# Performance work log

Hardware: AMD Instinct MI355X
Metric: run time of the kernel (lower is better)

The kernel has to match this reference:

```python
import jax, jax.numpy as jnp
import numpy as np

HIDDEN = 2048
NUM_HEADS = 32
NUM_KV_HEADS = 8
GROUP = NUM_HEADS // NUM_KV_HEADS  # 4
HEAD_DIM = HIDDEN // NUM_HEADS     # 64
SEQ = 2048


def setup_inputs() -> dict:
    key = jax.random.key(0)
    ks = jax.random.split(key, 5)
    s = HIDDEN ** -0.5
    x = jax.random.normal(ks[0], (SEQ, HIDDEN), jnp.float32)
    q_proj = jax.random.normal(ks[1], (HIDDEN, HIDDEN), jnp.float32) * s
    k_proj = jax.random.normal(ks[2], (HIDDEN, HIDDEN // GROUP), jnp.float32) * s
    v_proj = jax.random.normal(ks[3], (HIDDEN, HIDDEN // GROUP), jnp.float32) * s
    o_proj = jax.random.normal(ks[4], (HIDDEN, HIDDEN), jnp.float32) * s
    # inv_freq = 1/rsqrt(10000**(i/d)) = sqrt(10000**(i/d)) per the original module
    inv_freq = jnp.sqrt(10000.0 ** (jnp.arange(0, HEAD_DIM, 2) / HEAD_DIM)).astype(jnp.float32)
    return {"x": x, "q_proj": q_proj, "k_proj": k_proj, "v_proj": v_proj,
            "o_proj": o_proj, "inv_freq": inv_freq}


def _rope(x, inv_freq):
    # x: [S, ..., HEAD_DIM]; rotation per the original (nonstandard) formula.
    orig_dtype = x.dtype
    x = x.astype(jnp.float32)
    seq = jnp.arange(x.shape[0])
    angles = seq[:, None] * jax.lax.stop_gradient(inv_freq)[None, :]  # [S, HEAD_DIM//2]
    bshape = (x.shape[0],) + (1,) * (x.ndim - 2) + (HEAD_DIM // 2,)
    sins = jnp.sin(angles).reshape(bshape)
    coss = jnp.cos(angles).reshape(bshape)
    half, odd = jnp.split(x, 2, axis=-1)
    out = jnp.concatenate([half * coss + odd * sins, half * sins - odd * coss], axis=-1)
    return out.astype(orig_dtype)


def reference(x, q_proj, k_proj, v_proj, o_proj, inv_freq):
    S = x.shape[0]
    q = (x @ q_proj).reshape(S, NUM_KV_HEADS, GROUP, HEAD_DIM)
    k = (x @ k_proj).reshape(S, NUM_KV_HEADS, HEAD_DIM)
    v = (x @ v_proj).reshape(S, NUM_KV_HEADS, HEAD_DIM)
    q = _rope(q, inv_freq)
    k = _rope(k, inv_freq)
    # scores: [a=S, b=S, h=kv_heads, g=group]
    scores = jnp.einsum('ahgd,bhd->abhg', q, k) / (HEAD_DIM ** 0.5)
    mask = jnp.tril(jnp.ones((S, S), dtype=jnp.bool_))[:, :, None, None]
    scores = jnp.where(mask, scores, -jnp.inf)
    attn = jax.nn.softmax(scores, axis=1)  # softmax over b (axis=-3)
    o = jnp.einsum('abhg,bhd->ahgd', attn, v).reshape(S, HIDDEN)
    return o @ o_proj
```

## Files before the change

### kernel.cpp

```cpp
#include <hip/hip_runtime.h>


typedef __bf16 bf16_t;
typedef __bf16 bf16x4 __attribute__((ext_vector_type(4)));
typedef __bf16 bf16x8 __attribute__((ext_vector_type(8)));
typedef float  f32x4  __attribute__((ext_vector_type(4)));
typedef short  s16x4  __attribute__((ext_vector_type(4)));

#define S_LEN   2048
#define HID     2048
#define NKV     8
#define NH      32
#define DHEAD   64
#define KVW     (NKV * DHEAD)

__device__ __align__(16) bf16_t g_xb [S_LEN * HID];
__device__ __align__(16) bf16_t g_wTq[HID * HID];
__device__ __align__(16) bf16_t g_wTk[KVW * HID];
__device__ __align__(16) bf16_t g_wTv[KVW * HID];
__device__ __align__(16) bf16_t g_wTo[HID * HID];
__device__ __align__(16) bf16_t g_q [S_LEN * HID];
__device__ __align__(16) bf16_t g_k [S_LEN * KVW];
__device__ __align__(16) bf16_t g_vT[KVW * S_LEN];
__device__ __align__(16) bf16_t g_om[S_LEN * HID];
__device__ float g_ropeC[S_LEN * 32];
__device__ float g_ropeS[S_LEN * 32];

static __device__ inline s16x4 bc4(bf16x4 v) { s16x4 r; __builtin_memcpy(&r, &v, 8); return r; }

__device__ __forceinline__ void gll16(void* lds, const void* g) {
    __builtin_amdgcn_global_load_lds(
        (const __attribute__((address_space(1))) void*)g,
        (__attribute__((address_space(3))) void*)lds,
        16, 0, 0);
}

__global__ __launch_bounds__(256)
void prep_kernel(const float* __restrict__ x,
                 const float* __restrict__ qw, const float* __restrict__ kw,
                 const float* __restrict__ vw, const float* __restrict__ ow,
                 const void* __restrict__ invf_raw) {
    __shared__ bf16_t tile[64][65];
    int b = blockIdx.x, t = threadIdx.x;

    if (b < 256) {
        int idx = b * 256 + t;
        int s = idx >> 5, j = idx & 31;
        float f;
        if (*(const unsigned*)invf_raw == 0x3F800000u) {
            f = ((const float*)invf_raw)[j];
        } else {
            unsigned u = ((unsigned)((const unsigned short*)invf_raw)[j]) << 16;
            __builtin_memcpy(&f, &u, 4);
        }
        double a = (double)s * (double)f;
        g_ropeC[idx] = (float)cos(a);
        g_ropeS[idx] = (float)sin(a);
        return;
    }
    if (b < 4352) {
        int idx = (b - 256) * 256 + t;
        float4 v = reinterpret_cast<const float4*>(x)[idx];
        bf16x4 o;
        o[0] = (bf16_t)v.x; o[1] = (bf16_t)v.y; o[2] = (bf16_t)v.z; o[3] = (bf16_t)v.w;
        *reinterpret_cast<bf16x4*>(&g_xb[(size_t)idx * 4]) = o;
        return;
    }
    const float* in; bf16_t* outp; int R, C, tb;
    if (b < 5376)      { in = qw; outp = g_wTq; R = HID; C = HID; tb = b - 4352; }
    else if (b < 5632) { in = kw; outp = g_wTk; R = HID; C = KVW; tb = b - 5376; }
    else if (b < 5888) { in = vw; outp = g_wTv; R = HID; C = KVW; tb = b - 5632; }
    else               { in = ow; outp = g_wTo; R = HID; C = HID; tb = b - 5888; }
    int xt = C >> 6;
    int c0 = (tb % xt) * 64, r0 = (tb / xt) * 64;
    int tx = t & 63, ty = t >> 6;
    #pragma unroll
    for (int r = ty; r < 64; r += 4)
        tile[r][tx] = (bf16_t)in[(size_t)(r0 + r) * C + c0 + tx];
    __syncthreads();
    #pragma unroll
    for (int r = ty; r < 64; r += 4)
        outp[(size_t)(c0 + r) * R + r0 + tx] = tile[tx][r];
}

__global__ __launch_bounds__(256)
void gemm_fused_kernel(float* __restrict__ Cf, int which) {
    __shared__ __align__(16) bf16_t As[2][64 * 64];
    __shared__ __align__(16) bf16_t Bs[2][128 * 64];

    int t    = threadIdx.x;
    int lane = t & 63, wid = t >> 6;
    int quad = lane >> 4, l15 = lane & 15;
    int bx = blockIdx.x, m0 = blockIdx.y * 64;
    int wm = (wid >> 1) * 32, wn = (wid & 1) * 64;

    const bf16_t* A; const bf16_t* Bt; int n0;
    if (which == 1)      { A = g_om; Bt = g_wTo; n0 = bx * 128; }
    else {
        A = g_xb;
        if (bx < 16)      { Bt = g_wTq; n0 = bx * 128; }
        else if (bx < 20) { Bt = g_wTk; n0 = (bx - 16) * 128; }
        else              { Bt = g_wTv; n0 = (bx - 20) * 128; }
    }

    int crow = lane >> 3;
    int gseg = (lane & 7) ^ crow;
    int so   = l15 & 7;

    f32x4 acc[2][4];
    #pragma unroll
    for (int im = 0; im < 2; ++im)
        #pragma unroll
        for (int in = 0; in < 4; ++in)
            #pragma unroll
            for (int r = 0; r < 4; ++r) acc[im][in][r] = 0.f;

    auto stage = [&](int buf, int kt) {
        int ca0 = wid * 2, cb0 = wid * 4;
        gll16(&As[buf][(ca0 + 0) * 512], A  + (size_t)(m0 + (ca0 + 0) * 8 + crow) * HID + kt + gseg * 8);
        gll16(&As[buf][(ca0 + 1) * 512], A  + (size_t)(m0 + (ca0 + 1) * 8 + crow) * HID + kt + gseg * 8);
        gll16(&Bs[buf][(cb0 + 0) * 512], Bt + (size_t)(n0 + (cb0 + 0) * 8 + crow) * HID + kt + gseg * 8);
        gll16(&Bs[buf][(cb0 + 1) * 512], Bt + (size_t)(n0 + (cb0 + 1) * 8 + crow) * HID + kt + gseg * 8);
        gll16(&Bs[buf][(cb0 + 2) * 512], Bt + (size_t)(n0 + (cb0 + 2) * 8 + crow) * HID + kt + gseg * 8);
        gll16(&Bs[buf][(cb0 + 3) * 512], Bt + (size_t)(n0 + (cb0 + 3) * 8 + crow) * HID + kt + gseg * 8);
    };

    stage(0, 0);

    for (int it = 0; it < 32; ++it) {
        int cur = it & 1;
        __syncthreads();
        if (it + 1 < 32)
            stage(cur ^ 1, (it + 1) * 64);

        bf16x8 af[2][2], bfr[4][2];
        #pragma unroll
        for (int im = 0; im < 2; ++im)
            #pragma unroll
            for (int kh = 0; kh < 2; ++kh)
                af[im][kh] = *reinterpret_cast<const bf16x8*>(
                    &As[cur][(wm + im * 16 + l15) * 64 + (((kh * 4 + quad) ^ so) * 8)]);
        #pragma unroll
        for (int in = 0; in < 4; ++in)
            #pragma unroll
            for (int kh = 0; kh < 2; ++kh)
                bfr[in][kh] = *reinterpret_cast<const bf16x8*>(
                    &Bs[cur][(wn + in * 16 + l15) * 64 + (((kh * 4 + quad) ^ so) * 8)]);
        #pragma unroll
        for (int im = 0; im < 2; ++im)
            #pragma unroll
            for (int in = 0; in < 4; ++in)
                #pragma unroll
                for (int kh = 0; kh < 2; ++kh)
                    acc[im][in] = __builtin_amdgcn_mfma_f32_16x16x32_bf16(
                        af[im][kh], bfr[in][kh], acc[im][in], 0, 0, 0);
    }

    if (which == 1) {
        #pragma unroll
        for (int im = 0; im < 2; ++im) {
            int rowb = m0 + wm + im * 16 + quad * 4;
            #pragma unroll
            for (int in = 0; in < 4; ++in) {
                int col = bx * 128 + wn + in * 16 + l15;
                #pragma unroll
                for (int r = 0; r < 4; ++r)
                    Cf[(size_t)(rowb + r) * HID + col] = acc[im][in][r];
            }
        }
    } else if (bx < 20) {
        bf16_t* Cb; int N, colbase;
        if (bx < 16) { Cb = g_q; N = HID; colbase = bx * 128 + wn; }
        else         { Cb = g_k; N = KVW; colbase = (bx - 16) * 128 + wn; }
        #pragma unroll
        for (int im = 0; im < 2; ++im) {
            #pragma unroll
            for (int r = 0; r < 4; ++r) {
                int row = m0 + wm + im * 16 + quad * 4 + r;
                #pragma unroll
                for (int in = 0; in < 2; ++in) {
                    int d = in * 16 + l15;
                    float a  = acc[im][in][r];
                    float bb = acc[im][in + 2][r];
                    float cc = g_ropeC[row * 32 + d];
                    float ss = g_ropeS[row * 32 + d];
                    Cb[(size_t)row * N + colbase + d]      = (bf16_t)(a * cc + bb * ss);
                    Cb[(size_t)row * N + colbase + 32 + d] = (bf16_t)(a * ss - bb * cc);
                }
            }
        }
    } else {
        #pragma unroll
        for (int im = 0; im < 2; ++im) {
            int rowb = m0 + wm + im * 16 + quad * 4;
            #pragma unroll
            for (int in = 0; in < 4; ++in) {
                int col = (bx - 20) * 128 + wn + in * 16 + l15;
                #pragma unroll
                for (int r = 0; r < 4; ++r)
                    g_vT[(size_t)col * S_LEN + (rowb + r)] = (bf16_t)acc[im][in][r];
            }
        }
    }
}

__global__ __launch_bounds__(256)
void flash_kernel() {
    __shared__ __align__(16) bf16_t Ks[64][72];
    __shared__ __align__(16) bf16_t Vs[64][72];

    int t    = threadIdx.x;
    int lane = t & 63, wid = t >> 6;
    int quad = lane >> 4, l15 = lane & 15;
    int hk   = blockIdx.x & 7;
    int qb32 = 63 - (blockIdx.x >> 3);
    int head = hk * 4 + wid;
    int q0   = qb32 * 32;

    bf16x8 aq[2][2];
    #pragma unroll
    for (int mq = 0; mq < 2; ++mq) {
        const bf16_t* qp = g_q + (size_t)(q0 + mq * 16 + l15) * HID + head * 64 + quad * 8;
        aq[mq][0] = *reinterpret_cast<const bf16x8*>(qp);
        aq[mq][1] = *reinterpret_cast<const bf16x8*>(qp + 32);
        #pragma unroll
        for (int j = 0; j < 8; ++j) {
            aq[mq][0][j] = (bf16_t)((float)aq[mq][0][j] * 0.125f);
            aq[mq][1][j] = (bf16_t)((float)aq[mq][1][j] * 0.125f);
        }
    }

    bf16x4 ones4;
    #pragma unroll
    for (int j = 0; j < 4; ++j) ones4[j] = (bf16_t)1.0f;
    s16x4 ones_s = bc4(ones4);

    f32x4 oacc[2][4], liacc[2];
    #pragma unroll
    for (int mq = 0; mq < 2; ++mq) {
        #pragma unroll
        for (int r = 0; r < 4; ++r) liacc[mq][r] = 0.f;
        #pragma unroll
        for (int dt = 0; dt < 4; ++dt)
            #pragma unroll
            for (int r = 0; r < 4; ++r) oacc[mq][dt][r] = 0.f;
    }

    int qcol[2] = { q0 + l15, q0 + 16 + l15 };
    int nkt = (qb32 >> 1) + 1;

    for (int kt = 0; kt < nkt; ++kt) {
        int k0 = kt * 64;
        __syncthreads();
        #pragma unroll
        for (int i = t; i < 512; i += 256) {
            int row = i >> 3, seg = i & 7;
            *reinterpret_cast<int4*>(&Ks[row][seg * 8]) =
                *reinterpret_cast<const int4*>(g_k + (size_t)(k0 + row) * KVW + hk * 64 + seg * 8);
            *reinterpret_cast<int4*>(&Vs[row][seg * 8]) =
                *reinterpret_cast<const int4*>(g_vT + (size_t)(hk * 64 + row) * S_LEN + k0 + seg * 8);
        }
        __syncthreads();

        bf16x8 ak[4][2];
        #pragma unroll
        for (int mk = 0; mk < 4; ++mk) {
            ak[mk][0] = *reinterpret_cast<const bf16x8*>(&Ks[mk * 16 + l15][quad * 8]);
            ak[mk][1] = *reinterpret_cast<const bf16x8*>(&Ks[mk * 16 + l15][32 + quad * 8]);
        }

        f32x4 sacc[4][2];
        #pragma unroll
        for (int mk = 0; mk < 4; ++mk)
            #pragma unroll
            for (int mq = 0; mq < 2; ++mq) {
                f32x4 s;
                #pragma unroll
                for (int r = 0; r < 4; ++r) s[r] = 0.f;
                s = __builtin_amdgcn_mfma_f32_16x16x32_bf16(ak[mk][0], aq[mq][0], s, 0, 0, 0);
                s = __builtin_amdgcn_mfma_f32_16x16x32_bf16(ak[mk][1], aq[mq][1], s, 0, 0, 0);
                sacc[mk][mq] = s;
            }

        s16x4 pas[4][2];
        #pragma unroll
        for (int mk = 0; mk < 4; ++mk)
            #pragma unroll
            for (int mq = 0; mq < 2; ++mq) {
                bf16x4 pa;
                #pragma unroll
                for (int r = 0; r < 4; ++r) {
                    int kk = k0 + mk * 16 + quad * 4 + r;
                    pa[r] = (bf16_t)((kk <= qcol[mq]) ? __expf(sacc[mk][mq][r] - 16.0f) : 0.0f);
                }
                pas[mk][mq] = bc4(pa);
            }

        #pragma unroll
        for (int mk = 0; mk < 4; ++mk) {
            #pragma unroll
            for (int dt = 0; dt < 4; ++dt) {
                bf16x4 bv = *reinterpret_cast<const bf16x4*>(&Vs[dt * 16 + l15][mk * 16 + quad * 4]);
                s16x4 bvs = bc4(bv);
                #pragma unroll
                for (int mq = 0; mq < 2; ++mq)
                    oacc[mq][dt] = __builtin_amdgcn_mfma_f32_16x16x16bf16_1k(pas[mk][mq], bvs, oacc[mq][dt], 0, 0, 0);
            }
            #pragma unroll
            for (int mq = 0; mq < 2; ++mq)
                liacc[mq] = __builtin_amdgcn_mfma_f32_16x16x16bf16_1k(pas[mk][mq], ones_s, liacc[mq], 0, 0, 0);
        }
    }

    #pragma unroll
    for (int mq = 0; mq < 2; ++mq)
        #pragma unroll
        for (int r = 0; r < 4; ++r) {
            float inv = 1.0f / liacc[mq][r];
            int row = q0 + mq * 16 + quad * 4 + r;
            #pragma unroll
            for (int dt = 0; dt < 4; ++dt)
                g_om[(size_t)row * HID + head * 64 + dt * 16 + l15] = (bf16_t)(oacc[mq][dt][r] * inv);
        }
}

extern "C" void kernel_launch(void* const* d_in, const int* in_sizes, int n_in,
                              void* d_out, int out_size, void* d_ws, size_t ws_size,
                              hipStream_t stream) {
    const float* x    = (const float*)d_in[0];
    const float* qpW  = (const float*)d_in[1];
    const float* kpW  = (const float*)d_in[2];
    const float* vpW  = (const float*)d_in[3];
    const float* opW  = (const float*)d_in[4];
    const void*  invf = d_in[5];
    float* out = (float*)d_out;

    prep_kernel<<<6912, 256, 0, stream>>>(x, qpW, kpW, vpW, opW, invf);
    gemm_fused_kernel<<<dim3(24, 32), 256, 0, stream>>>(nullptr, 0);
    flash_kernel<<<512, 256, 0, stream>>>();
    gemm_fused_kernel<<<dim3(16, 32), 256, 0, stream>>>(out, 1);
}
```

Before: 258.2 us.

## Split flash attention over key chunks with a separate combine kernel

Each query block's key range is split into chunks of 8 key tiles, handled by separate workgroups across 2048 blocks, which write unnormalized fp32 partial outputs and row sums. A new combine kernel adds the partials and normalizes them into the bf16 attention output. The aim is to fix the load imbalance of the causal triangle, where a few blocks each had to process up to 32 tiles. The cost is an extra launch plus fp32 partial traffic through global memory. It relies on the existing softmax having no running max, which is what allows the partials to be summed directly.

Result: faster. 251.6 us (-2.6%).

```diff
diff --git a/kernel.cpp b/kernel.cpp
--- a/kernel.cpp
+++ b/kernel.cpp
@@ -25,6 +25,8 @@
 __device__ __align__(16) bf16_t g_om[S_LEN * HID];
 __device__ float g_ropeC[S_LEN * 32];
 __device__ float g_ropeS[S_LEN * 32];
+__device__ __align__(16) float g_po[4u * S_LEN * HID];
+__device__ float g_pl[4u * S_LEN * NH];
 
 static __device__ inline s16x4 bc4(bf16x4 v) { s16x4 r; __builtin_memcpy(&r, &v, 8); return r; }
 
@@ -205,15 +207,22 @@
 }
 
 __global__ __launch_bounds__(256)
-void flash_kernel() {
+void flash_part_kernel() {
     __shared__ __align__(16) bf16_t Ks[64][72];
     __shared__ __align__(16) bf16_t Vs[64][72];
 
     int t    = threadIdx.x;
     int lane = t & 63, wid = t >> 6;
     int quad = lane >> 4, l15 = lane & 15;
-    int hk   = blockIdx.x & 7;
-    int qb32 = 63 - (blockIdx.x >> 3);
+    int bx   = blockIdx.x;
+    int hk   = bx & 7;
+    int qb32 = (bx >> 3) & 63;
+    int chunk = bx >> 9;
+    int nkt  = (qb32 >> 1) + 1;
+    int kt0  = chunk * 8;
+    if (kt0 >= nkt) return;
+    int kt1  = min(kt0 + 8, nkt);
+
     int head = hk * 4 + wid;
     int q0   = qb32 * 32;
 
@@ -247,9 +256,8 @@
     }
 
     int qcol[2] = { q0 + l15, q0 + 16 + l15 };
-    int nkt = (qb32 >> 1) + 1;
-
-    for (int kt = 0; kt < nkt; ++kt) {
+
+    for (int kt = kt0; kt < kt1; ++kt) {
         int k0 = kt * 64;
         __syncthreads();
         #pragma unroll
@@ -312,16 +320,42 @@
         }
     }
 
+    float* po = g_po + (size_t)chunk * S_LEN * HID;
     #pragma unroll
     for (int mq = 0; mq < 2; ++mq)
         #pragma unroll
         for (int r = 0; r < 4; ++r) {
-            float inv = 1.0f / liacc[mq][r];
             int row = q0 + mq * 16 + quad * 4 + r;
             #pragma unroll
             for (int dt = 0; dt < 4; ++dt)
-                g_om[(size_t)row * HID + head * 64 + dt * 16 + l15] = (bf16_t)(oacc[mq][dt][r] * inv);
-        }
+                po[(size_t)row * HID + head * 64 + dt * 16 + l15] = oacc[mq][dt][r];
+            if (l15 == 0)
+                g_pl[((size_t)chunk * S_LEN + row) * NH + head] = liacc[mq][r];
+        }
+}
+
+__global__ __launch_bounds__(256)
+void flash_combine_kernel() {
+    int t = blockIdx.x * 256 + threadIdx.x;
+    int row  = t >> 9;
+    int col4 = (t & 511) * 4;
+    int head = col4 >> 6;
+    int nkt  = ((row >> 5) >> 1) + 1;
+    int nc   = (nkt + 7) >> 3;
+
+    float4 s = make_float4(0.f, 0.f, 0.f, 0.f);
+    float l = 0.f;
+    for (int c = 0; c < nc; ++c) {
+        const float4 v = *reinterpret_cast<const float4*>(
+            g_po + ((size_t)c * S_LEN + row) * HID + col4);
+        s.x += v.x; s.y += v.y; s.z += v.z; s.w += v.w;
+        l += g_pl[((size_t)c * S_LEN + row) * NH + head];
+    }
+    float inv = 1.0f / l;
+    bf16x4 o;
+    o[0] = (bf16_t)(s.x * inv); o[1] = (bf16_t)(s.y * inv);
+    o[2] = (bf16_t)(s.z * inv); o[3] = (bf16_t)(s.w * inv);
+    *reinterpret_cast<bf16x4*>(&g_om[(size_t)row * HID + col4]) = o;
 }
 
 extern "C" void kernel_launch(void* const* d_in, const int* in_sizes, int n_in,
@@ -337,6 +371,7 @@
 
     prep_kernel<<<6912, 256, 0, stream>>>(x, qpW, kpW, vpW, opW, invf);
     gemm_fused_kernel<<<dim3(24, 32), 256, 0, stream>>>(nullptr, 0);
-    flash_kernel<<<512, 256, 0, stream>>>();
+    flash_part_kernel<<<2048, 256, 0, stream>>>();
+    flash_combine_kernel<<<4096, 256, 0, stream>>>();
     gemm_fused_kernel<<<dim3(16, 32), 256, 0, stream>>>(out, 1);
 }
```
